# Optimization experiments

Measured on AMD Instinct MI355X. Metric: run time of the kernel, lower is better.

The kernel has to match this reference:

```python
import jax, jax.numpy as jnp
import numpy as np

NUM_FIELDS = 32
BATCH = 16384
EMBED_DIM = 64

# static pair index lists, exactly as built in __init__
_pairs = np.array([(i, j) for i in range(NUM_FIELDS - 1) for j in range(i + 1, NUM_FIELDS)], dtype=np.int32)
ROW = jnp.asarray(_pairs[:, 0])  # [P] with P = F*(F-1)/2 = 496
COL = jnp.asarray(_pairs[:, 1])


def setup_inputs() -> dict:
    key = jax.random.key(0)
    x = jax.random.normal(key, (BATCH, NUM_FIELDS, EMBED_DIM), dtype=jnp.float32)
    return {"x": x}


def reference(x):
    # Original: pq[b,k] = sum_{a,b'} p[b,k,a] * q[b,k,b']  (full outer product summed)
    # which is algebraically identical to sum_a(p) * sum_b(q).
    s = jnp.sum(x, axis=-1)          # [B, F]
    return s[:, ROW] * s[:, COL]      # [B, P]
```

## Files before the change

### kernel.cpp

```cpp
#include <hip/hip_runtime.h>

#define NUM_FIELDS 32
#define EMBED_DIM  64
#define NUM_PAIRS  496

struct Pairs {
    unsigned char r[NUM_PAIRS];
    unsigned char c[NUM_PAIRS];
};
constexpr Pairs make_pairs() {
    Pairs t{};
    int p = 0;
    for (int i = 0; i < NUM_FIELDS - 1; ++i)
        for (int j = i + 1; j < NUM_FIELDS; ++j) {
            t.r[p] = (unsigned char)i;
            t.c[p] = (unsigned char)j;
            ++p;
        }
    return t;
}
__device__ constexpr Pairs PAIRS = make_pairs();

__global__ __launch_bounds__(256)
void opn_kernel(const float* __restrict__ x, float* __restrict__ out, int batch) {
    const int b = blockIdx.x;
    if (b >= batch) return;
    const int t = threadIdx.x;

    __shared__ float s_sh[NUM_FIELDS];

    const float4* __restrict__ x4 =
        (const float4*)(x + (size_t)b * NUM_FIELDS * EMBED_DIM);

    float4 a = x4[t];
    float4 c = x4[256 + t];
    float p1 = (a.x + a.y) + (a.z + a.w);
    float p2 = (c.x + c.y) + (c.z + c.w);

    #pragma unroll
    for (int off = 8; off >= 1; off >>= 1) {
        p1 += __shfl_xor(p1, off);
        p2 += __shfl_xor(p2, off);
    }

    if ((t & 15) == 0) {
        const int f = t >> 4;
        s_sh[f]      = p1;
        s_sh[16 + f] = p2;
    }
    __syncthreads();

    if (t < NUM_PAIRS / 4) {
        const int p0 = t * 4;
        float4 r;
        r.x = s_sh[PAIRS.r[p0 + 0]] * s_sh[PAIRS.c[p0 + 0]];
        r.y = s_sh[PAIRS.r[p0 + 1]] * s_sh[PAIRS.c[p0 + 1]];
        r.z = s_sh[PAIRS.r[p0 + 2]] * s_sh[PAIRS.c[p0 + 2]];
        r.w = s_sh[PAIRS.r[p0 + 3]] * s_sh[PAIRS.c[p0 + 3]];
        ((float4*)(out + (size_t)b * NUM_PAIRS))[t] = r;
    }
}

extern "C" void kernel_launch(void* const* d_in, const int* in_sizes, int n_in,
                              void* d_out, int out_size, void* d_ws, size_t ws_size,
                              hipStream_t stream) {
    const float* x = (const float*)d_in[0];
    float* out = (float*)d_out;
    const int batch = in_sizes[0] / (NUM_FIELDS * EMBED_DIM);
    opn_kernel<<<batch, 256, 0, stream>>>(x, out, batch);
}
```

Measured before the change: 193.2 us.

## Process eight batch rows per block with nontemporal loads and stores

Each block now handles eight batch rows instead of one. It issues all sixteen float4 loads up front for memory-level parallelism and writes the pair products with a strided loop covering every output element. Loads and stores use nontemporal builtins to bypass cache retention for streaming data. The block count drops eightfold and register pressure rises. There is no tail guard for batches that are not a multiple of eight.

```diff
diff --git a/kernel.cpp b/kernel.cpp
--- a/kernel.cpp
+++ b/kernel.cpp
@@ -3,6 +3,10 @@
 #define NUM_FIELDS 32
 #define EMBED_DIM  64
 #define NUM_PAIRS  496
+#define ROWS       8
+#define P4         (NUM_PAIRS / 4)
+
+typedef float f4 __attribute__((ext_vector_type(4)));
 
 struct Pairs {
     unsigned char r[NUM_PAIRS];
@@ -23,41 +27,50 @@
 
 __global__ __launch_bounds__(256)
 void opn_kernel(const float* __restrict__ x, float* __restrict__ out, int batch) {
-    const int b = blockIdx.x;
-    if (b >= batch) return;
     const int t = threadIdx.x;
+    const int row0 = blockIdx.x * ROWS;
+    if (row0 >= batch) return;
 
-    __shared__ float s_sh[NUM_FIELDS];
+    __shared__ float s_sh[ROWS][NUM_FIELDS];
 
-    const float4* __restrict__ x4 =
-        (const float4*)(x + (size_t)b * NUM_FIELDS * EMBED_DIM);
+    const f4* __restrict__ x4 =
+        (const f4*)(x + (size_t)row0 * NUM_FIELDS * EMBED_DIM);
 
-    float4 a = x4[t];
-    float4 c = x4[256 + t];
-    float p1 = (a.x + a.y) + (a.z + a.w);
-    float p2 = (c.x + c.y) + (c.z + c.w);
+    f4 a[ROWS], c[ROWS];
+    #pragma unroll
+    for (int r = 0; r < ROWS; ++r) {
+        a[r] = __builtin_nontemporal_load(&x4[r * 512 + t]);
+        c[r] = __builtin_nontemporal_load(&x4[r * 512 + 256 + t]);
+    }
 
     #pragma unroll
-    for (int off = 8; off >= 1; off >>= 1) {
-        p1 += __shfl_xor(p1, off);
-        p2 += __shfl_xor(p2, off);
-    }
-
-    if ((t & 15) == 0) {
-        const int f = t >> 4;
-        s_sh[f]      = p1;
-        s_sh[16 + f] = p2;
+    for (int r = 0; r < ROWS; ++r) {
+        float p1 = (a[r].x + a[r].y) + (a[r].z + a[r].w);
+        float p2 = (c[r].x + c[r].y) + (c[r].z + c[r].w);
+        #pragma unroll
+        for (int off = 8; off >= 1; off >>= 1) {
+            p1 += __shfl_xor(p1, off);
+            p2 += __shfl_xor(p2, off);
+        }
+        if ((t & 15) == 0) {
+            const int f = t >> 4;
+            s_sh[r][f]      = p1;
+            s_sh[r][16 + f] = p2;
+        }
     }
     __syncthreads();
 
-    if (t < NUM_PAIRS / 4) {
-        const int p0 = t * 4;
-        float4 r;
-        r.x = s_sh[PAIRS.r[p0 + 0]] * s_sh[PAIRS.c[p0 + 0]];
-        r.y = s_sh[PAIRS.r[p0 + 1]] * s_sh[PAIRS.c[p0 + 1]];
-        r.z = s_sh[PAIRS.r[p0 + 2]] * s_sh[PAIRS.c[p0 + 2]];
-        r.w = s_sh[PAIRS.r[p0 + 3]] * s_sh[PAIRS.c[p0 + 3]];
-        ((float4*)(out + (size_t)b * NUM_PAIRS))[t] = r;
+    f4* __restrict__ o4 = (f4*)(out + (size_t)row0 * NUM_PAIRS);
+    #pragma unroll
+    for (int i = t; i < ROWS * P4; i += 256) {
+        const int r  = i / P4;
+        const int p0 = (i - r * P4) * 4;
+        f4 v;
+        v.x = s_sh[r][PAIRS.r[p0 + 0]] * s_sh[r][PAIRS.c[p0 + 0]];
+        v.y = s_sh[r][PAIRS.r[p0 + 1]] * s_sh[r][PAIRS.c[p0 + 1]];
+        v.z = s_sh[r][PAIRS.r[p0 + 2]] * s_sh[r][PAIRS.c[p0 + 2]];
+        v.w = s_sh[r][PAIRS.r[p0 + 3]] * s_sh[r][PAIRS.c[p0 + 3]];
+        __builtin_nontemporal_store(v, &o4[i]);
     }
 }
 
@@ -67,5 +80,6 @@
     const float* x = (const float*)d_in[0];
     float* out = (float*)d_out;
     const int batch = in_sizes[0] / (NUM_FIELDS * EMBED_DIM);
-    opn_kernel<<<batch, 256, 0, stream>>>(x, out, batch);
+    const int grid = (batch + ROWS - 1) / ROWS;
+    opn_kernel<<<grid, 256, 0, stream>>>(x, out, batch);
 }
```

New measurement: 189.3 us. -2.0%, faster.
